# Optimization experiments

Measured on AMD Instinct MI355X. Metric: run time of the kernel, lower is better.

## Reference

```python
import jax, jax.numpy as jnp
import numpy as np

K_HEADS = 8
D_HEAD = 8
C_IN = 128   # c_x + c_t after channel concat
C_OUT = K_HEADS * D_HEAD  # 64
SMALL = -32767.0  # -2**15 + 1


def setup_inputs() -> dict:
    key = jax.random.key(0)
    ks = jax.random.split(key, 12)
    B, Cx, V, T = 8, 64, 200, 128
    x = jax.random.normal(ks[0], (B, Cx, V, T), dtype=jnp.float32)
    tem_embedding = jax.random.normal(ks[1], (B, Cx, V, T), dtype=jnp.float32)
    s = 0.05
    Wq = jax.random.normal(ks[2], (C_OUT, C_IN), dtype=jnp.float32) * s
    bq = jax.random.normal(ks[3], (C_OUT,), dtype=jnp.float32) * s
    Wk = jax.random.normal(ks[4], (C_OUT, C_IN), dtype=jnp.float32) * s
    bk = jax.random.normal(ks[5], (C_OUT,), dtype=jnp.float32) * s
    Wv = jax.random.normal(ks[6], (C_OUT, C_IN), dtype=jnp.float32) * s
    bv = jax.random.normal(ks[7], (C_OUT,), dtype=jnp.float32) * s
    Wo = jax.random.normal(ks[8], (C_OUT, C_OUT), dtype=jnp.float32) * s
    bo = jax.random.normal(ks[9], (C_OUT,), dtype=jnp.float32) * s
    return {"x": x, "tem_embedding": tem_embedding,
            "Wq": Wq, "bq": bq, "Wk": Wk, "bk": bk,
            "Wv": Wv, "bv": bv, "Wo": Wo, "bo": bo}


def reference(x, tem_embedding, Wq, bq, Wk, bk, Wv, bv, Wo, bo):
    B, _, V, T = x.shape
    # concat temporal embedding on channel dim (last T steps)
    xt = jnp.concatenate([x, tem_embedding[:, :, :, -T:]], axis=1)  # [B, C_IN, V, T]

    def proj(W, b):  # 1x1 conv == channel einsum
        return jnp.einsum('oi,bivt->bovt', W, xt) + b[None, :, None, None]

    def heads(t):  # [B, K*d, V, T] -> [K*B, V, T, d] (split on dim1, cat on dim0)
        t = t.reshape(B, K_HEADS, D_HEAD, V, T)
        t = jnp.transpose(t, (1, 0, 3, 4, 2))  # [K, B, V, T, d]
        return t.reshape(K_HEADS * B, V, T, D_HEAD)

    q = heads(proj(Wq, bq))
    k = heads(proj(Wk, bk))
    v = heads(proj(Wv, bv))

    attn = jnp.einsum('nvtd,nvsd->nvts', q, k) / jnp.sqrt(jnp.float32(D_HEAD))
    causal = jnp.tril(jnp.ones((T, T), dtype=bool))  # [T, T]
    attn = jnp.where(causal[None, None, :, :], attn, SMALL)
    attn = jax.nn.softmax(attn, axis=-1)
    out = jnp.einsum('nvts,nvsd->nvtd', attn, v)  # [K*B, V, T, d]

    # merge heads back: [K*B, V, T, d] -> [B, K*d, V, T]
    out = out.reshape(K_HEADS, B, V, T, D_HEAD)
    out = jnp.transpose(out, (1, 0, 4, 2, 3)).reshape(B, K_HEADS * D_HEAD, V, T)
    out = jnp.einsum('oi,bivt->bovt', Wo, out) + bo[None, :, None, None]
    return jax.nn.relu(out)
```

## Files before the change

kernel.cpp:

```cpp
#include <hip/hip_runtime.h>
#include <stdint.h>

#define TPB 512

constexpr int Bb   = 8;
constexpr int Vv   = 200;
constexpr int Tt   = 128;
constexpr int CIN  = 128;
constexpr int COUT = 64;

typedef __attribute__((ext_vector_type(8))) short bf16x8;
typedef __attribute__((ext_vector_type(4))) short short4v;
typedef __attribute__((ext_vector_type(4))) float f32x4;

__device__ __forceinline__ unsigned short f2bf(float f) {
    union { float f; unsigned u; } x; x.f = f;
    unsigned r = x.u + 0x7fffu + ((x.u >> 16) & 1u);
    return (unsigned short)(r >> 16);
}
__device__ __forceinline__ unsigned pk2(float a, float b) {
    return (unsigned)f2bf(a) | ((unsigned)f2bf(b) << 16);
}

#if __has_builtin(__builtin_amdgcn_mfma_f32_16x16x16bf16_1k)
#define MFMA16(a, b, c) __builtin_amdgcn_mfma_f32_16x16x16bf16_1k(a, b, c, 0, 0, 0)
#else
__device__ __forceinline__ f32x4 mfma16_asm(short4v a, short4v b, f32x4 c) {
    f32x4 d;
    asm("v_mfma_f32_16x16x16_bf16 %0, %1, %2, %3" : "=v"(d) : "v"(a), "v"(b), "v"(c));
    return d;
}
#define MFMA16(a, b, c) mfma16_asm(a, b, c)
#endif

__global__ __launch_bounds__(TPB, 6)
void tatt_fused(const float* __restrict__ x, const float* __restrict__ tem,
                const float* __restrict__ Wq, const float* __restrict__ bq,
                const float* __restrict__ Wk, const float* __restrict__ bk,
                const float* __restrict__ Wv, const float* __restrict__ bv,
                const float* __restrict__ Wo, const float* __restrict__ bo,
                float* __restrict__ out)
{
    __shared__ __align__(16) unsigned char smem[53248];
    unsigned short* qk = (unsigned short*)smem;
    unsigned short* vt = (unsigned short*)(smem + 32768);
    unsigned short* ot = (unsigned short*)(smem + 32768);
    unsigned short* xt = (unsigned short*)(smem + 49152);

    const int tid = threadIdx.x;
    const int w = tid >> 6, lane = tid & 63;
    const int l15 = lane & 15, qd = lane >> 4;
    const int b = blockIdx.x / Vv, v = blockIdx.x % Vv;
    const float QS = 1.44269504088896f * 0.35355339059327f;

    bf16x8 afr0[4], afr1[4];
    {
        const float* W0 = (w < 4) ? Wq : Wv;
        const int o0_ = (w < 4) ? w : (w - 4);
        const float* base0 = W0 + (o0_ * 16 + l15) * CIN + qd * 8;
        #pragma unroll
        for (int kc = 0; kc < 4; ++kc) {
            float4 fa = *(const float4*)(base0 + kc * 32);
            float4 fb = *(const float4*)(base0 + kc * 32 + 4);
            union { bf16x8 v8; unsigned u[4]; } t;
            t.u[0] = pk2(fa.x, fa.y); t.u[1] = pk2(fa.z, fa.w);
            t.u[2] = pk2(fb.x, fb.y); t.u[3] = pk2(fb.z, fb.w);
            afr0[kc] = t.v8;
        }
        if (w < 4) {
            const float* base1 = Wk + (w * 16 + l15) * CIN + qd * 8;
            #pragma unroll
            for (int kc = 0; kc < 4; ++kc) {
                float4 fa = *(const float4*)(base1 + kc * 32);
                float4 fb = *(const float4*)(base1 + kc * 32 + 4);
                union { bf16x8 v8; unsigned u[4]; } t;
                t.u[0] = pk2(fa.x, fa.y); t.u[1] = pk2(fa.z, fa.w);
                t.u[2] = pk2(fb.x, fb.y); t.u[3] = pk2(fb.z, fb.w);
                afr1[kc] = t.v8;
            }
        }
    }

    auto tileC = [&](const bf16x8 (&A)[4], int p, int ot_, int r) {
        f32x4 acc = {0.f, 0.f, 0.f, 0.f};
        const unsigned short* Bbp = xt + l15 * CIN;
        #pragma unroll
        for (int kc = 0; kc < 4; ++kc) {
            int phys = (kc * 4 + qd) ^ l15;
            bf16x8 bb = *(const bf16x8*)(Bbp + phys * 8);
            acc = __builtin_amdgcn_mfma_f32_16x16x32_bf16(A[kc], bb, acc, 0, 0, 0);
        }
        const int obase = ot_ * 16 + qd * 4;
        const float* bp = (p == 0) ? bq : ((p == 1) ? bk : bv);
        float4 bias = *(const float4*)(bp + obase);
        float bb4[4] = {bias.x, bias.y, bias.z, bias.w};
        const int tg = r * 16 + l15;
        if (p == 2) {
            #pragma unroll
            for (int rr = 0; rr < 4; ++rr) {
                int dg = obase + rr;
                int tp = tg ^ ((((dg >> 2) & 3)) << 4);
                vt[dg * 128 + tp] = f2bf(acc[rr] + bb4[rr]);
            }
        } else {
            float sc = (p == 0) ? QS : 1.0f;
            ushort4 s4;
            s4.x = f2bf((acc[0] + bb4[0]) * sc);
            s4.y = f2bf((acc[1] + bb4[1]) * sc);
            s4.z = f2bf((acc[2] + bb4[2]) * sc);
            s4.w = f2bf((acc[3] + bb4[3]) * sc);
            int phys = (obase >> 2) ^ (tg & 14);
            *(ushort4*)(qk + p * 8192 + tg * 64 + phys * 4) = s4;
        }
    };

    {
        const int sc_ = tid >> 2;
        const int stq = tid & 3;
        const float* sbase = (sc_ < 64 ? x : tem)
            + ((b * 64 + (sc_ & 63)) * Vv + v) * Tt + stq * 4;
        float4 pf = *(const float4*)(sbase);
        const int clow = sc_ & 7, chi = sc_ >> 3;

        for (int r = 0; r < 8; ++r) {
            if (r) __syncthreads();
            {
                int t0 = stq * 4;
                xt[(t0 + 0) * CIN + ((chi ^ (t0 + 0)) << 3) + clow] = f2bf(pf.x);
                xt[(t0 + 1) * CIN + ((chi ^ (t0 + 1)) << 3) + clow] = f2bf(pf.y);
                xt[(t0 + 2) * CIN + ((chi ^ (t0 + 2)) << 3) + clow] = f2bf(pf.z);
                xt[(t0 + 3) * CIN + ((chi ^ (t0 + 3)) << 3) + clow] = f2bf(pf.w);
            }
            if (r < 7) pf = *(const float4*)(sbase + (r + 1) * 16);
            __syncthreads();
            if (w < 4) { tileC(afr0, 0, w, r); tileC(afr1, 1, w, r); }
            else       { tileC(afr0, 2, w - 4, r); }
        }
    }
    __syncthreads();

    {
        const int h = w;
        short4v vfrag[8];
        {
            const int dg = h * 8 + l15;
            const int swz = ((dg >> 2) & 3) << 4;
            #pragma unroll
            for (int st = 0; st < 8; ++st) {
                short4v f = {0, 0, 0, 0};
                if (l15 < 8) {
                    int sp = (st * 16 + qd * 4) ^ swz;
                    f = *(const short4v*)(vt + dg * 128 + sp);
                }
                vfrag[st] = f;
            }
        }
        __syncthreads();

        bool dmask[4];
        #pragma unroll
        for (int r = 0; r < 4; ++r) dmask[r] = (qd * 4 + r) <= l15;
        const int qkoff = ((h * 2 + qd) ^ (l15 & 14)) << 2;

        #pragma unroll
        for (int tt = 0; tt < 8; ++tt) {
            short4v qf = {0, 0, 0, 0};
            if (qd < 2) qf = *(const short4v*)(qk + (tt * 16 + l15) * 64 + qkoff);
            f32x4 o0 = {0.f, 0.f, 0.f, 0.f}, o1 = {0.f, 0.f, 0.f, 0.f};
            float lac = 0.f;
            #pragma unroll
            for (int st = 0; st < 8; ++st) {
                if (st <= tt) {
                    short4v kf = {0, 0, 0, 0};
                    if (qd < 2) kf = *(const short4v*)(qk + 8192 + (st * 16 + l15) * 64 + qkoff);
                    f32x4 z = {0.f, 0.f, 0.f, 0.f};
                    f32x4 s = MFMA16(kf, qf, z);
                    float p0 = __builtin_amdgcn_exp2f(s[0]);
                    float p1 = __builtin_amdgcn_exp2f(s[1]);
                    float p2 = __builtin_amdgcn_exp2f(s[2]);
                    float p3 = __builtin_amdgcn_exp2f(s[3]);
                    if (st == tt) {
                        p0 = dmask[0] ? p0 : 0.f;
                        p1 = dmask[1] ? p1 : 0.f;
                        p2 = dmask[2] ? p2 : 0.f;
                        p3 = dmask[3] ? p3 : 0.f;
                    }
                    lac += (p0 + p1) + (p2 + p3);
                    int pp0 = (int)pk2(p0, p1), pp1 = (int)pk2(p2, p3);
                    short4v pf;
                    pf[0] = (short)(pp0 & 0xffff); pf[1] = (short)(pp0 >> 16);
                    pf[2] = (short)(pp1 & 0xffff); pf[3] = (short)(pp1 >> 16);
                    if (st & 1) o1 = MFMA16(vfrag[st], pf, o1);
                    else        o0 = MFMA16(vfrag[st], pf, o0);
                }
            }
            float l = lac;
            l += __shfl_xor(l, 16, 64);
            l += __shfl_xor(l, 32, 64);
            float rl = __builtin_amdgcn_rcpf(l);
            if (qd < 2) {
                float r0 = (o0[0] + o1[0]) * rl, r1 = (o0[1] + o1[1]) * rl;
                float r2 = (o0[2] + o1[2]) * rl, r3 = (o0[3] + o1[3]) * rl;
                int t = tt * 16 + l15;
                uint2 st2;
                st2.x = pk2(r0, r1);
                st2.y = pk2(r2, r3);
                *(uint2*)(ot + t * 64 + (((h * 2 + qd) ^ (l15 & 14)) << 2)) = st2;
            }
        }
    }
    __syncthreads();

    {
        const int tq3 = w & 3, ohB = (w >> 2) * 2;
        bf16x8 wof[2][2];
        #pragma unroll
        for (int oth = 0; oth < 2; ++oth) {
            const float* base = Wo + ((ohB + oth) * 16 + l15) * COUT + qd * 8;
            #pragma unroll
            for (int kc = 0; kc < 2; ++kc) {
                float4 fa = *(const float4*)(base + kc * 32);
                float4 fb = *(const float4*)(base + kc * 32 + 4);
                union { bf16x8 v8; unsigned u[4]; } t;
                t.u[0] = pk2(fa.x, fa.y); t.u[1] = pk2(fa.z, fa.w);
                t.u[2] = pk2(fb.x, fb.y); t.u[3] = pk2(fb.z, fb.w);
                wof[oth][kc] = t.v8;
            }
        }
        #pragma unroll
        for (int ts = 0; ts < 2; ++ts) {
            const int tt = tq3 * 2 + ts;
            #pragma unroll
            for (int oth = 0; oth < 2; ++oth) {
                const int ot_ = ohB + oth;
                f32x4 acc = {0.f, 0.f, 0.f, 0.f};
                #pragma unroll
                for (int kc = 0; kc < 2; ++kc) {
                    bf16x8 bb = *(const bf16x8*)(ot + (tt * 16 + l15) * 64
                                     + (((kc * 8 + qd * 2) ^ (l15 & 14)) << 2));
                    acc = __builtin_amdgcn_mfma_f32_16x16x32_bf16(wof[oth][kc], bb, acc, 0, 0, 0);
                }
                const int obase = ot_ * 16 + qd * 4;
                float4 bias = *(const float4*)(bo + obase);
                const int t = tt * 16 + l15;
                float vr[4] = {acc[0] + bias.x, acc[1] + bias.y,
                               acc[2] + bias.z, acc[3] + bias.w};
                #pragma unroll
                for (int r = 0; r < 4; ++r) {
                    float val = vr[r];
                    out[((b * COUT + obase + r) * Vv + v) * Tt + t] = val > 0.f ? val : 0.f;
                }
            }
        }
    }
}

extern "C" void kernel_launch(void* const* d_in, const int* in_sizes, int n_in,
                              void* d_out, int out_size, void* d_ws, size_t ws_size,
                              hipStream_t stream) {
    (void)in_sizes; (void)n_in; (void)ws_size; (void)out_size; (void)d_ws;
    const float* x   = (const float*)d_in[0];
    const float* tem = (const float*)d_in[1];
    const float* Wq  = (const float*)d_in[2];
    const float* bq  = (const float*)d_in[3];
    const float* Wk  = (const float*)d_in[4];
    const float* bk  = (const float*)d_in[5];
    const float* Wv  = (const float*)d_in[6];
    const float* bv  = (const float*)d_in[7];
    const float* Wo  = (const float*)d_in[8];
    const float* bo  = (const float*)d_in[9];
    float* out = (float*)d_out;

    tatt_fused<<<dim3(Bb * Vv), dim3(TPB), 0, stream>>>(
        x, tem, Wq, bq, Wk, bk, Wv, bv, Wo, bo, out);
}
```

Baseline: 224.4 us.

## Interleave projection, causal attention and output projection per time tile

```diff
diff --git a/kernel.cpp b/kernel.cpp
--- a/kernel.cpp
+++ b/kernel.cpp
@@ -33,7 +33,7 @@
 #define MFMA16(a, b, c) mfma16_asm(a, b, c)
 #endif
 
-__global__ __launch_bounds__(TPB, 6)
+__global__ __launch_bounds__(TPB, 8)
 void tatt_fused(const float* __restrict__ x, const float* __restrict__ tem,
                 const float* __restrict__ Wq, const float* __restrict__ bq,
                 const float* __restrict__ Wk, const float* __restrict__ bk,
@@ -41,11 +41,12 @@
                 const float* __restrict__ Wo, const float* __restrict__ bo,
                 float* __restrict__ out)
 {
-    __shared__ __align__(16) unsigned char smem[53248];
-    unsigned short* qk = (unsigned short*)smem;
-    unsigned short* vt = (unsigned short*)(smem + 32768);
-    unsigned short* ot = (unsigned short*)(smem + 32768);
-    unsigned short* xt = (unsigned short*)(smem + 49152);
+    __shared__ __align__(16) unsigned char smem[40960];
+    unsigned short* kbuf = (unsigned short*)smem;
+    unsigned short* vt   = (unsigned short*)(smem + 16384);
+    unsigned short* xt   = (unsigned short*)(smem + 32768);
+    unsigned short* qbuf = (unsigned short*)(smem + 36864);
+    unsigned short* obuf = (unsigned short*)(smem + 38912);
 
     const int tid = threadIdx.x;
     const int w = tid >> 6, lane = tid & 63;
@@ -53,11 +54,16 @@
     const int b = blockIdx.x / Vv, v = blockIdx.x % Vv;
     const float QS = 1.44269504088896f * 0.35355339059327f;
 
+    const int ot_   = w & 3;
+    const int obase = ot_ * 16 + qd * 4;
+    const int qkoff = ((w * 2 + qd) ^ (l15 & 14)) << 2;
+    const int vdg   = w * 8 + l15;
+    const int vswz  = ((vdg >> 2) & 3) << 4;
+
     bf16x8 afr0[4], afr1[4];
     {
         const float* W0 = (w < 4) ? Wq : Wv;
-        const int o0_ = (w < 4) ? w : (w - 4);
-        const float* base0 = W0 + (o0_ * 16 + l15) * CIN + qd * 8;
+        const float* base0 = W0 + (ot_ * 16 + l15) * CIN + qd * 8;
         #pragma unroll
         for (int kc = 0; kc < 4; ++kc) {
             float4 fa = *(const float4*)(base0 + kc * 32);
@@ -68,7 +74,7 @@
             afr0[kc] = t.v8;
         }
         if (w < 4) {
-            const float* base1 = Wk + (w * 16 + l15) * CIN + qd * 8;
+            const float* base1 = Wk + (ot_ * 16 + l15) * CIN + qd * 8;
             #pragma unroll
             for (int kc = 0; kc < 4; ++kc) {
                 float4 fa = *(const float4*)(base1 + kc * 32);
@@ -78,10 +84,21 @@
                 t.u[2] = pk2(fb.x, fb.y); t.u[3] = pk2(fb.z, fb.w);
                 afr1[kc] = t.v8;
             }
+        } else {
+            const float* baseO = Wo + (ot_ * 16 + l15) * COUT + qd * 8;
+            #pragma unroll
+            for (int kc = 0; kc < 2; ++kc) {
+                float4 fa = *(const float4*)(baseO + kc * 32);
+                float4 fb = *(const float4*)(baseO + kc * 32 + 4);
+                union { bf16x8 v8; unsigned u[4]; } t;
+                t.u[0] = pk2(fa.x, fa.y); t.u[1] = pk2(fa.z, fa.w);
+                t.u[2] = pk2(fb.x, fb.y); t.u[3] = pk2(fb.z, fb.w);
+                afr1[kc] = t.v8;
+            }
         }
     }
 
-    auto tileC = [&](const bf16x8 (&A)[4], int p, int ot_, int r) {
+    auto projTile = [&](const bf16x8 (&A)[4], int p, const float* bp, int r) {
         f32x4 acc = {0.f, 0.f, 0.f, 0.f};
         const unsigned short* Bbp = xt + l15 * CIN;
         #pragma unroll
@@ -90,169 +107,131 @@
             bf16x8 bb = *(const bf16x8*)(Bbp + phys * 8);
             acc = __builtin_amdgcn_mfma_f32_16x16x32_bf16(A[kc], bb, acc, 0, 0, 0);
         }
-        const int obase = ot_ * 16 + qd * 4;
-        const float* bp = (p == 0) ? bq : ((p == 1) ? bk : bv);
         float4 bias = *(const float4*)(bp + obase);
         float bb4[4] = {bias.x, bias.y, bias.z, bias.w};
-        const int tg = r * 16 + l15;
         if (p == 2) {
+            int tg = r * 16 + l15;
             #pragma unroll
             for (int rr = 0; rr < 4; ++rr) {
                 int dg = obase + rr;
                 int tp = tg ^ ((((dg >> 2) & 3)) << 4);
                 vt[dg * 128 + tp] = f2bf(acc[rr] + bb4[rr]);
             }
+        } else if (p == 1) {
+            int tg = r * 16 + l15;
+            ushort4 s4;
+            s4.x = f2bf(acc[0] + bb4[0]); s4.y = f2bf(acc[1] + bb4[1]);
+            s4.z = f2bf(acc[2] + bb4[2]); s4.w = f2bf(acc[3] + bb4[3]);
+            int phys = (obase >> 2) ^ (tg & 14);
+            *(ushort4*)(kbuf + tg * 64 + phys * 4) = s4;
         } else {
-            float sc = (p == 0) ? QS : 1.0f;
             ushort4 s4;
-            s4.x = f2bf((acc[0] + bb4[0]) * sc);
-            s4.y = f2bf((acc[1] + bb4[1]) * sc);
-            s4.z = f2bf((acc[2] + bb4[2]) * sc);
-            s4.w = f2bf((acc[3] + bb4[3]) * sc);
-            int phys = (obase >> 2) ^ (tg & 14);
-            *(ushort4*)(qk + p * 8192 + tg * 64 + phys * 4) = s4;
+            s4.x = f2bf((acc[0] + bb4[0]) * QS); s4.y = f2bf((acc[1] + bb4[1]) * QS);
+            s4.z = f2bf((acc[2] + bb4[2]) * QS); s4.w = f2bf((acc[3] + bb4[3]) * QS);
+            int phys = (obase >> 2) ^ (l15 & 14);
+            *(ushort4*)(qbuf + l15 * 64 + phys * 4) = s4;
         }
     };
 
+    auto oproj = [&](int tile) {
+        f32x4 acc = {0.f, 0.f, 0.f, 0.f};
+        #pragma unroll
+        for (int kc = 0; kc < 2; ++kc) {
+            bf16x8 bb = *(const bf16x8*)(obuf + l15 * 64
+                             + (((kc * 8 + qd * 2) ^ (l15 & 14)) << 2));
+            acc = __builtin_amdgcn_mfma_f32_16x16x32_bf16(afr1[kc], bb, acc, 0, 0, 0);
+        }
+        float4 bias = *(const float4*)(bo + obase);
+        int t = tile * 16 + l15;
+        float vr[4] = {acc[0] + bias.x, acc[1] + bias.y,
+                       acc[2] + bias.z, acc[3] + bias.w};
+        #pragma unroll
+        for (int rr = 0; rr < 4; ++rr) {
+            float val = vr[rr];
+            out[((b * COUT + obase + rr) * Vv + v) * Tt + t] = val > 0.f ? val : 0.f;
+        }
+    };
+
+    const int sc_ = tid >> 2, stq = tid & 3;
+    const float* sbase = (sc_ < 64 ? x : tem)
+        + ((b * 64 + (sc_ & 63)) * Vv + v) * Tt + stq * 4;
+    const int clow = sc_ & 7, chi = sc_ >> 3;
+
+    float4 pf = *(const float4*)sbase;
     {
-        const int sc_ = tid >> 2;
-        const int stq = tid & 3;
-        const float* sbase = (sc_ < 64 ? x : tem)
-            + ((b * 64 + (sc_ & 63)) * Vv + v) * Tt + stq * 4;
-        float4 pf = *(const float4*)(sbase);
-        const int clow = sc_ & 7, chi = sc_ >> 3;
-
-        for (int r = 0; r < 8; ++r) {
-            if (r) __syncthreads();
-            {
-                int t0 = stq * 4;
-                xt[(t0 + 0) * CIN + ((chi ^ (t0 + 0)) << 3) + clow] = f2bf(pf.x);
-                xt[(t0 + 1) * CIN + ((chi ^ (t0 + 1)) << 3) + clow] = f2bf(pf.y);
-                xt[(t0 + 2) * CIN + ((chi ^ (t0 + 2)) << 3) + clow] = f2bf(pf.z);
-                xt[(t0 + 3) * CIN + ((chi ^ (t0 + 3)) << 3) + clow] = f2bf(pf.w);
-            }
-            if (r < 7) pf = *(const float4*)(sbase + (r + 1) * 16);
-            __syncthreads();
-            if (w < 4) { tileC(afr0, 0, w, r); tileC(afr1, 1, w, r); }
-            else       { tileC(afr0, 2, w - 4, r); }
-        }
+        int t0 = stq * 4;
+        xt[(t0 + 0) * CIN + ((chi ^ (t0 + 0)) << 3) + clow] = f2bf(pf.x);
+        xt[(t0 + 1) * CIN + ((chi ^ (t0 + 1)) << 3) + clow] = f2bf(pf.y);
+        xt[(t0 + 2) * CIN + ((chi ^ (t0 + 2)) << 3) + clow] = f2bf(pf.z);
+        xt[(t0 + 3) * CIN + ((chi ^ (t0 + 3)) << 3) + clow] = f2bf(pf.w);
     }
+    pf = *(const float4*)(sbase + 16);
     __syncthreads();
 
-    {
-        const int h = w;
-        short4v vfrag[8];
-        {
-            const int dg = h * 8 + l15;
-            const int swz = ((dg >> 2) & 3) << 4;
-            #pragma unroll
-            for (int st = 0; st < 8; ++st) {
-                short4v f = {0, 0, 0, 0};
-                if (l15 < 8) {
-                    int sp = (st * 16 + qd * 4) ^ swz;
-                    f = *(const short4v*)(vt + dg * 128 + sp);
-                }
-                vfrag[st] = f;
-            }
+    for (int r = 0; r < 8; ++r) {
+        if (w < 4) {
+            projTile(afr0, 0, bq, r);
+            projTile(afr1, 1, bk, r);
+        } else {
+            projTile(afr0, 2, bv, r);
+            if (r > 0) oproj(r - 1);
         }
         __syncthreads();
 
-        bool dmask[4];
-        #pragma unroll
-        for (int r = 0; r < 4; ++r) dmask[r] = (qd * 4 + r) <= l15;
-        const int qkoff = ((h * 2 + qd) ^ (l15 & 14)) << 2;
-
-        #pragma unroll
-        for (int tt = 0; tt < 8; ++tt) {
-            short4v qf = {0, 0, 0, 0};
-            if (qd < 2) qf = *(const short4v*)(qk + (tt * 16 + l15) * 64 + qkoff);
-            f32x4 o0 = {0.f, 0.f, 0.f, 0.f}, o1 = {0.f, 0.f, 0.f, 0.f};
-            float lac = 0.f;
-            #pragma unroll
-            for (int st = 0; st < 8; ++st) {
-                if (st <= tt) {
-                    short4v kf = {0, 0, 0, 0};
-                    if (qd < 2) kf = *(const short4v*)(qk + 8192 + (st * 16 + l15) * 64 + qkoff);
-                    f32x4 z = {0.f, 0.f, 0.f, 0.f};
-                    f32x4 s = MFMA16(kf, qf, z);
-                    float p0 = __builtin_amdgcn_exp2f(s[0]);
-                    float p1 = __builtin_amdgcn_exp2f(s[1]);
-                    float p2 = __builtin_amdgcn_exp2f(s[2]);
-                    float p3 = __builtin_amdgcn_exp2f(s[3]);
-                    if (st == tt) {
-                        p0 = dmask[0] ? p0 : 0.f;
-                        p1 = dmask[1] ? p1 : 0.f;
-                        p2 = dmask[2] ? p2 : 0.f;
-                        p3 = dmask[3] ? p3 : 0.f;
-                    }
-                    lac += (p0 + p1) + (p2 + p3);
-                    int pp0 = (int)pk2(p0, p1), pp1 = (int)pk2(p2, p3);
-                    short4v pf;
-                    pf[0] = (short)(pp0 & 0xffff); pf[1] = (short)(pp0 >> 16);
-                    pf[2] = (short)(pp1 & 0xffff); pf[3] = (short)(pp1 >> 16);
-                    if (st & 1) o1 = MFMA16(vfrag[st], pf, o1);
-                    else        o0 = MFMA16(vfrag[st], pf, o0);
-                }
-            }
-            float l = lac;
-            l += __shfl_xor(l, 16, 64);
-            l += __shfl_xor(l, 32, 64);
-            float rl = __builtin_amdgcn_rcpf(l);
-            if (qd < 2) {
-                float r0 = (o0[0] + o1[0]) * rl, r1 = (o0[1] + o1[1]) * rl;
-                float r2 = (o0[2] + o1[2]) * rl, r3 = (o0[3] + o1[3]) * rl;
-                int t = tt * 16 + l15;
-                uint2 st2;
-                st2.x = pk2(r0, r1);
-                st2.y = pk2(r2, r3);
-                *(uint2*)(ot + t * 64 + (((h * 2 + qd) ^ (l15 & 14)) << 2)) = st2;
-            }
-        }
+        if (r < 7) {
+            int t0 = stq * 4;
+            xt[(t0 + 0) * CIN + ((chi ^ (t0 + 0)) << 3) + clow] = f2bf(pf.x);
+            xt[(t0 + 1) * CIN + ((chi ^ (t0 + 1)) << 3) + clow] = f2bf(pf.y);
+            xt[(t0 + 2) * CIN + ((chi ^ (t0 + 2)) << 3) + clow] = f2bf(pf.z);
+            xt[(t0 + 3) * CIN + ((chi ^ (t0 + 3)) << 3) + clow] = f2bf(pf.w);
+        }
+        if (r < 6) pf = *(const float4*)(sbase + (r + 2) * 16);
+
+        short4v qf = {0, 0, 0, 0};
+        if (qd < 2) qf = *(const short4v*)(qbuf + l15 * 64 + qkoff);
+        f32x4 o0 = {0.f, 0.f, 0.f, 0.f}, o1 = {0.f, 0.f, 0.f, 0.f};
+        float lac = 0.f;
+        for (int st = 0; st <= r; ++st) {
+            short4v kf = {0, 0, 0, 0};
+            if (qd < 2) kf = *(const short4v*)(kbuf + (st * 16 + l15) * 64 + qkoff);
+            short4v vf = {0, 0, 0, 0};
+            if (l15 < 8) vf = *(const short4v*)(vt + vdg * 128 + ((st * 16 + qd * 4) ^ vswz));
+            f32x4 z = {0.f, 0.f, 0.f, 0.f};
+            f32x4 s = MFMA16(kf, qf, z);
+            float p0 = __builtin_amdgcn_exp2f(s[0]);
+            float p1 = __builtin_amdgcn_exp2f(s[1]);
+            float p2 = __builtin_amdgcn_exp2f(s[2]);
+            float p3 = __builtin_amdgcn_exp2f(s[3]);
+            if (st == r) {
+                p0 = (qd * 4 + 0) <= l15 ? p0 : 0.f;
+                p1 = (qd * 4 + 1) <= l15 ? p1 : 0.f;
+                p2 = (qd * 4 + 2) <= l15 ? p2 : 0.f;
+                p3 = (qd * 4 + 3) <= l15 ? p3 : 0.f;
+            }
+            lac += (p0 + p1) + (p2 + p3);
+            int pp0 = (int)pk2(p0, p1), pp1 = (int)pk2(p2, p3);
+            short4v pfv;
+            pfv[0] = (short)(pp0 & 0xffff); pfv[1] = (short)(pp0 >> 16);
+            pfv[2] = (short)(pp1 & 0xffff); pfv[3] = (short)(pp1 >> 16);
+            if (st & 1) o1 = MFMA16(vf, pfv, o1);
+            else        o0 = MFMA16(vf, pfv, o0);
+        }
+        float l = lac;
+        l += __shfl_xor(l, 16, 64);
+        l += __shfl_xor(l, 32, 64);
+        float rl = __builtin_amdgcn_rcpf(l);
+        if (qd < 2) {
+            float r0 = (o0[0] + o1[0]) * rl, r1 = (o0[1] + o1[1]) * rl;
+            float r2 = (o0[2] + o1[2]) * rl, r3 = (o0[3] + o1[3]) * rl;
+            uint2 st2;
+            st2.x = pk2(r0, r1);
+            st2.y = pk2(r2, r3);
+            *(uint2*)(obuf + l15 * 64 + qkoff) = st2;
+        }
+        __syncthreads();
     }
-    __syncthreads();
-
-    {
-        const int tq3 = w & 3, ohB = (w >> 2) * 2;
-        bf16x8 wof[2][2];
-        #pragma unroll
-        for (int oth = 0; oth < 2; ++oth) {
-            const float* base = Wo + ((ohB + oth) * 16 + l15) * COUT + qd * 8;
-            #pragma unroll
-            for (int kc = 0; kc < 2; ++kc) {
-                float4 fa = *(const float4*)(base + kc * 32);
-                float4 fb = *(const float4*)(base + kc * 32 + 4);
-                union { bf16x8 v8; unsigned u[4]; } t;
-                t.u[0] = pk2(fa.x, fa.y); t.u[1] = pk2(fa.z, fa.w);
-                t.u[2] = pk2(fb.x, fb.y); t.u[3] = pk2(fb.z, fb.w);
-                wof[oth][kc] = t.v8;
-            }
-        }
-        #pragma unroll
-        for (int ts = 0; ts < 2; ++ts) {
-            const int tt = tq3 * 2 + ts;
-            #pragma unroll
-            for (int oth = 0; oth < 2; ++oth) {
-                const int ot_ = ohB + oth;
-                f32x4 acc = {0.f, 0.f, 0.f, 0.f};
-                #pragma unroll
-                for (int kc = 0; kc < 2; ++kc) {
-                    bf16x8 bb = *(const bf16x8*)(ot + (tt * 16 + l15) * 64
-                                     + (((kc * 8 + qd * 2) ^ (l15 & 14)) << 2));
-                    acc = __builtin_amdgcn_mfma_f32_16x16x32_bf16(wof[oth][kc], bb, acc, 0, 0, 0);
-                }
-                const int obase = ot_ * 16 + qd * 4;
-                float4 bias = *(const float4*)(bo + obase);
-                const int t = tt * 16 + l15;
-                float vr[4] = {acc[0] + bias.x, acc[1] + bias.y,
-                               acc[2] + bias.z, acc[3] + bias.w};
-                #pragma unroll
-                for (int r = 0; r < 4; ++r) {
-                    float val = vr[r];
-                    out[((b * COUT + obase + r) * Vv + v) * Tt + t] = val > 0.f ? val : 0.f;
-                }
-            }
-        }
-    }
+
+    if (w >= 4) oproj(7);
 }
 
 extern "C" void kernel_launch(void* const* d_in, const int* in_sizes, int n_in,
```

New measurement: 322.7 us. +43.8%, slower.
